# Optimization experiments

Measured on AMD Instinct MI355X. Metric: run time of the kernel, lower is better.

## Reference

```python
import jax, jax.numpy as jnp
import numpy as np

# Module config (matches init_kwargs shape_data=[8,32,32], pow=1, spde_type='adv_diff')
N_T, N_Y, N_X = 8, 32, 32
N = N_Y * N_X            # nb_nodes
DX = DY = DT = 1.0


def build_A(kappa, m1, m2, h11, h12, h22):
    """Dense [N,N] advection-diffusion operator A = kappa^2 I + m.grad - div(H grad),
    central differences on the n_y x n_x grid, zero-Dirichlet boundary (9-pt stencil).
    All coefficient inputs are [N] vectors (node-wise)."""
    ii, jj = jnp.divmod(jnp.arange(N), N_X)   # ii: y index, jj: x index
    rows = jnp.arange(N)
    A = jnp.zeros((N, N), dtype=kappa.dtype)
    # center
    A = A.at[rows, rows].add(kappa ** 2 + 2.0 * h11 / DX**2 + 2.0 * h22 / DY**2)

    def add(A, di, dj, coef):
        vi, vj = ii + di, jj + dj
        valid = (vi >= 0) & (vi < N_Y) & (vj >= 0) & (vj < N_X)
        cols = jnp.clip(vi, 0, N_Y - 1) * N_X + jnp.clip(vj, 0, N_X - 1)
        return A.at[rows, cols].add(jnp.where(valid, coef, 0.0))

    A = add(A, 0, +1, -h11 / DX**2 + m1 / (2.0 * DX))
    A = add(A, 0, -1, -h11 / DX**2 - m1 / (2.0 * DX))
    A = add(A, +1, 0, -h22 / DY**2 + m2 / (2.0 * DY))
    A = add(A, -1, 0, -h22 / DY**2 - m2 / (2.0 * DY))
    cxy = h12 / (2.0 * DX * DY)    # cross term -2*H12*u_xy with /(4 dx dy) stencil
    A = add(A, +1, +1, -cxy)
    A = add(A, -1, -1, -cxy)
    A = add(A, +1, -1, +cxy)
    A = add(A, -1, +1, +cxy)
    return A


def _forward(kappa, m, H, tau):
    n_b = kappa.shape[0]
    # reorder field params to [n_b, n_t, N]
    kap = jnp.moveaxis(kappa[:, 0], -1, 1)
    m1 = jnp.moveaxis(m[:, 0], -1, 1)
    m2 = jnp.moveaxis(m[:, 1], -1, 1)
    h11 = jnp.moveaxis(H[:, 0, 0], -1, 1)
    h12 = jnp.moveaxis(H[:, 0, 1], -1, 1)
    h22 = jnp.moveaxis(H[:, 1, 1], -1, 1)
    tau_ = jnp.moveaxis(tau[:, 0], -1, 1)

    flat = lambda a: a.reshape(n_b * N_T, N)
    A = jax.vmap(build_A)(flat(kap), flat(m1), flat(m2), flat(h11), flat(h12), flat(h22))
    A = A.reshape(n_b, N_T, N, N)                 # B = A since pow == 1

    eye = jnp.eye(N, dtype=A.dtype)
    M = eye + DT * A                               # inv_M_k = I + dt*B_k, [n_b,n_t,N,N]
    w = DT / (tau_ ** 2)                           # Qs_tilde_k = diag(dt / tau_k^2)

    WM = w[..., :, None] * M                       # diag(w_k) @ M_k
    P = jnp.einsum('btij,btik->btjk', M, WM)       # M_k^T diag(w_k) M_k

    # diagonal blocks: D_k = P_k + diag(w_{k+1}) for k < n_t-1; D_{n_t-1} = P_{n_t-1}
    w_next = jnp.concatenate([w[:, 1:], jnp.zeros_like(w[:, :1])], axis=1)
    D = P + w_next[..., :, None] * eye

    # sub-diagonal block (k, k-1) = -M_k^T diag(w_k), k = 1..n_t-1 (0-block padded at front)
    zblk = jnp.zeros((n_b, 1, N, N), dtype=A.dtype)
    lower = jnp.concatenate([zblk, -jnp.swapaxes(WM[:, 1:], -1, -2)], axis=1)
    # super-diagonal block (k, k+1) = -diag(w_{k+1}) M_{k+1}, k = 0..n_t-2 (0-block at end)
    upper = jnp.concatenate([-WM[:, 1:], zblk], axis=1)

    # block-tridiagonal precision Q, packed as [n_b, 3(diag,lower,upper), n_t, N, N]
    return jnp.stack([D, lower, upper], axis=1)


def setup_inputs() -> dict:
    key = jax.random.key(0)
    ks = jax.random.split(key, 4)
    n_b = 2
    kappa = 0.1 + 0.9 * jax.random.uniform(ks[0], (n_b, 1, N, N_T), dtype=jnp.float32)
    m = 0.2 * jax.random.normal(ks[1], (n_b, 2, N, N_T), dtype=jnp.float32)
    H = jax.random.uniform(ks[2], (n_b, 2, 2, N, N_T), dtype=jnp.float32)
    H = H.at[:, 0, 1].multiply(0.2)
    H = H.at[:, 1, 0].set(H[:, 0, 1])              # symmetric diffusion tensor
    tau = 0.5 + jax.random.uniform(ks[3], (n_b, 1, N, N_T), dtype=jnp.float32)
    return {"kappa": kappa, "m": m, "H": H, "tau": tau}


def reference(kappa, m, H, tau):
    return _forward(kappa, m, H, tau)
```

## Files before the change

kernel.cpp:

```cpp
#include <hip/hip_runtime.h>

#define NT 8
#define NY 32
#define NX 32
#define NN 1024

__device__ __forceinline__ void node_coefs(const float* __restrict__ kap,
                                           const float* __restrict__ m,
                                           const float* __restrict__ H,
                                           const float* __restrict__ tau,
                                           int b, int node, int tc,
                                           int iy, int ix,
                                           float* c , float& w) {
    const int base = node * NT + tc;
    const float kp  = kap[(b * NN) * NT + base];
    const float m1  = m[((b * 2 + 0) * NN) * NT + base];
    const float m2  = m[((b * 2 + 1) * NN) * NT + base];
    const float h11 = H[((b * 4 + 0) * NN) * NT + base];
    const float h12 = H[((b * 4 + 1) * NN) * NT + base];
    const float h22 = H[((b * 4 + 3) * NN) * NT + base];
    const float tv  = tau[(b * NN) * NT + base];
    w = 1.0f / (tv * tv);

    const float cxy = 0.5f * h12;
    const bool ym = iy > 0, yp = iy < NY - 1;
    const bool xm = ix > 0, xp = ix < NX - 1;

    c[4] = 1.0f + kp * kp + 2.0f * h11 + 2.0f * h22;
    c[0] = (ym && xm) ? -cxy               : 0.0f;
    c[1] =  ym        ? (-h22 - 0.5f * m2) : 0.0f;
    c[2] = (ym && xp) ?  cxy               : 0.0f;
    c[3] =  xm        ? (-h11 - 0.5f * m1) : 0.0f;
    c[5] =  xp        ? (-h11 + 0.5f * m1) : 0.0f;
    c[6] = (yp && xm) ?  cxy               : 0.0f;
    c[7] =  yp        ? (-h22 + 0.5f * m2) : 0.0f;
    c[8] = (yp && xp) ? -cxy               : 0.0f;
}

__global__ __launch_bounds__(256) void spde_kernel(const float* __restrict__ kap,
                                                   const float* __restrict__ m,
                                                   const float* __restrict__ H,
                                                   const float* __restrict__ tau,
                                                   float* __restrict__ out) {
    __shared__ float sc[9][9];
    __shared__ float sw[9];
    __shared__ float valsD[25];
    __shared__ float valsL[9];
    __shared__ float valsU[9];

    const int gb = blockIdx.x;
    const int j  = gb & (NN - 1);
    const int bt = gb >> 10;
    const int t  = bt & 7;
    const int b  = bt >> 3;
    const int jy = j >> 5, jx = j & 31;
    const int tid = threadIdx.x;

    if (tid < 9) {
        const int ey = tid / 3 - 1, ex = tid % 3 - 1;
        const int iy = jy + ey, ix = jx + ex;
        float c[9];
        float w = 0.0f;
        if (iy >= 0 && iy < NY && ix >= 0 && ix < NX) {
            node_coefs(kap, m, H, tau, b, iy * NX + ix, t, iy, ix, c, w);
        } else {
            #pragma unroll
            for (int q = 0; q < 9; ++q) c[q] = 0.0f;
        }
        #pragma unroll
        for (int q = 0; q < 9; ++q) sc[tid][q] = c[q];
        sw[tid] = w;
    }
    __syncthreads();

    if (tid < 25) {
        const int dy = tid / 5 - 2, dx = tid % 5 - 2;
        float acc = 0.0f;
        #pragma unroll
        for (int d = 0; d < 9; ++d) {
            const int ey = d / 3 - 1, ex = d % 3 - 1;
            const int r2y = dy - ey, r2x = dx - ex;
            if (r2y >= -1 && r2y <= 1 && r2x >= -1 && r2x <= 1) {
                acc += sw[d] * sc[d][8 - d] * sc[d][(r2y + 1) * 3 + (r2x + 1)];
            }
        }
        if (tid == 12 && t < NT - 1) {
            const float tv = tau[((size_t)b * NN + j) * NT + (t + 1)];
            acc += 1.0f / (tv * tv);
        }
        valsD[tid] = acc;
    } else if (tid >= 64 && tid < 73) {
        const int d = tid - 64;
        valsL[d] = -sw[d] * sc[d][8 - d];
    } else if (tid >= 73 && tid < 82) {
        const int q = tid - 73;
        valsU[q] = -sw[4] * sc[4][q];
    }
    __syncthreads();

    const int cy  = tid >> 3;
    const int cx0 = (tid & 7) * 4;
    const int ddy = cy - jy;
    float4* const outq = (float4*)out;
    const size_t rowq = ((size_t)j << 8) + tid;
    const size_t matD = ((size_t)(b * 3 + 0) * NT + t) << 18;
    const size_t matL = ((size_t)(b * 3 + 1) * NT + t) << 18;

    {
        float4 v = make_float4(0.f, 0.f, 0.f, 0.f);
        if (ddy >= -2 && ddy <= 2) {
            float* vp = &v.x;
            const float* wrow = &valsD[(ddy + 2) * 5 + 2];
            #pragma unroll
            for (int qq = 0; qq < 4; ++qq) {
                const int ddx = cx0 + qq - jx;
                if (ddx >= -2 && ddx <= 2) vp[qq] = wrow[ddx];
            }
        }
        outq[matD + rowq] = v;
    }
    {
        float4 v = make_float4(0.f, 0.f, 0.f, 0.f);
        if (t > 0 && ddy >= -1 && ddy <= 1) {
            float* vp = &v.x;
            const float* wrow = &valsL[(ddy + 1) * 3 + 1];
            #pragma unroll
            for (int qq = 0; qq < 4; ++qq) {
                const int ddx = cx0 + qq - jx;
                if (ddx >= -1 && ddx <= 1) vp[qq] = wrow[ddx];
            }
        }
        outq[matL + rowq] = v;
    }
    if (t >= 1) {
        const size_t matU = ((size_t)(b * 3 + 2) * NT + (t - 1)) << 18;
        float4 v = make_float4(0.f, 0.f, 0.f, 0.f);
        if (ddy >= -1 && ddy <= 1) {
            float* vp = &v.x;
            const float* wrow = &valsU[(ddy + 1) * 3 + 1];
            #pragma unroll
            for (int qq = 0; qq < 4; ++qq) {
                const int ddx = cx0 + qq - jx;
                if (ddx >= -1 && ddx <= 1) vp[qq] = wrow[ddx];
            }
        }
        outq[matU + rowq] = v;
        if (t == NT - 1) {
            const size_t matU7 = ((size_t)(b * 3 + 2) * NT + 7) << 18;
            outq[matU7 + rowq] = make_float4(0.f, 0.f, 0.f, 0.f);
        }
    }
}

extern "C" void kernel_launch(void* const* d_in, const int* in_sizes, int n_in,
                              void* d_out, int out_size, void* d_ws, size_t ws_size,
                              hipStream_t stream) {
    const float* kap = (const float*)d_in[0];
    const float* m   = (const float*)d_in[1];
    const float* H   = (const float*)d_in[2];
    const float* tau = (const float*)d_in[3];
    float* out = (float*)d_out;

    const int n_b = in_sizes[0] / (NN * NT);
    const int grid = n_b * NT * NN;
    spde_kernel<<<grid, 256, 0, stream>>>(kap, m, H, tau, out);
}
```

Baseline: 199.3 us.

## Process a full grid row per block to reuse neighbor coefficients

Each block now handles a whole row of 32 output rows (one jy slab) instead of a single matrix row, loading a 3x32 halo of node coefficients once into shared memory. Per-row stencil weights are computed for all 32 columns and each thread writes 32 float4 stores per matrix in a loop. This cuts the launch count by 32x and removes the redundant coefficient loads repeated by neighboring blocks, in exchange for fewer blocks (512) and more serial store work per thread. The U block for t=0 now writes zeros into slot NT-1 through the same loop.

```diff
diff --git a/kernel.cpp b/kernel.cpp
--- a/kernel.cpp
+++ b/kernel.cpp
@@ -37,64 +37,63 @@
     c[8] = (yp && xp) ? -cxy               : 0.0f;
 }
 
-__global__ __launch_bounds__(256) void spde_kernel(const float* __restrict__ kap,
+__global__ __launch_bounds__(256) void slab_kernel(const float* __restrict__ kap,
                                                    const float* __restrict__ m,
                                                    const float* __restrict__ H,
                                                    const float* __restrict__ tau,
                                                    float* __restrict__ out) {
-    __shared__ float sc[9][9];
-    __shared__ float sw[9];
-    __shared__ float valsD[25];
-    __shared__ float valsL[9];
-    __shared__ float valsU[9];
+    __shared__ float sc[96][9];
+    __shared__ float sw[96];
+    __shared__ float valsD[32][25];
+    __shared__ float valsU[32][9];
 
-    const int gb = blockIdx.x;
-    const int j  = gb & (NN - 1);
-    const int bt = gb >> 10;
-    const int t  = bt & 7;
-    const int b  = bt >> 3;
-    const int jy = j >> 5, jx = j & 31;
+    const int blk = blockIdx.x;
+    const int jy = blk & 31;
+    const int t  = (blk >> 5) & 7;
+    const int b  = blk >> 8;
     const int tid = threadIdx.x;
 
-    if (tid < 9) {
-        const int ey = tid / 3 - 1, ex = tid % 3 - 1;
-        const int iy = jy + ey, ix = jx + ex;
-        float c[9];
+    if (tid < 96) {
+        const int r = tid >> 5;
+        const int c = tid & 31;
+        const int iy = jy - 1 + r;
+        float cf[9];
         float w = 0.0f;
-        if (iy >= 0 && iy < NY && ix >= 0 && ix < NX) {
-            node_coefs(kap, m, H, tau, b, iy * NX + ix, t, iy, ix, c, w);
+        if (iy >= 0 && iy < NY) {
+            node_coefs(kap, m, H, tau, b, iy * NX + c, t, iy, c, cf, w);
         } else {
             #pragma unroll
-            for (int q = 0; q < 9; ++q) c[q] = 0.0f;
+            for (int q = 0; q < 9; ++q) cf[q] = 0.0f;
         }
         #pragma unroll
-        for (int q = 0; q < 9; ++q) sc[tid][q] = c[q];
+        for (int q = 0; q < 9; ++q) sc[tid][q] = cf[q];
         sw[tid] = w;
     }
     __syncthreads();
 
-    if (tid < 25) {
-        const int dy = tid / 5 - 2, dx = tid % 5 - 2;
+    for (int e = tid; e < 32 * 25; e += 256) {
+        const int jx = e / 25, widx = e % 25;
+        const int dy = widx / 5 - 2, dx = widx % 5 - 2;
         float acc = 0.0f;
         #pragma unroll
         for (int d = 0; d < 9; ++d) {
             const int ey = d / 3 - 1, ex = d % 3 - 1;
             const int r2y = dy - ey, r2x = dx - ex;
-            if (r2y >= -1 && r2y <= 1 && r2x >= -1 && r2x <= 1) {
-                acc += sw[d] * sc[d][8 - d] * sc[d][(r2y + 1) * 3 + (r2x + 1)];
-            }
+            if (r2y < -1 || r2y > 1 || r2x < -1 || r2x > 1) continue;
+            const int col = jx + ex;
+            if ((unsigned)col >= 32u) continue;
+            const int i = (ey + 1) * 32 + col;
+            acc += sw[i] * sc[i][8 - d] * sc[i][(r2y + 1) * 3 + (r2x + 1)];
         }
-        if (tid == 12 && t < NT - 1) {
-            const float tv = tau[((size_t)b * NN + j) * NT + (t + 1)];
+        if (widx == 12 && t < NT - 1) {
+            const float tv = tau[((size_t)b * NN + jy * NX + jx) * NT + (t + 1)];
             acc += 1.0f / (tv * tv);
         }
-        valsD[tid] = acc;
-    } else if (tid >= 64 && tid < 73) {
-        const int d = tid - 64;
-        valsL[d] = -sw[d] * sc[d][8 - d];
-    } else if (tid >= 73 && tid < 82) {
-        const int q = tid - 73;
-        valsU[q] = -sw[4] * sc[4][q];
+        valsD[jx][widx] = acc;
+    }
+    for (int e = tid; e < 32 * 9; e += 256) {
+        const int jx = e / 9, off = e % 9;
+        valsU[jx][off] = -sw[32 + jx] * sc[32 + jx][off];
     }
     __syncthreads();
 
@@ -102,52 +101,73 @@
     const int cx0 = (tid & 7) * 4;
     const int ddy = cy - jy;
     float4* const outq = (float4*)out;
-    const size_t rowq = ((size_t)j << 8) + tid;
-    const size_t matD = ((size_t)(b * 3 + 0) * NT + t) << 18;
-    const size_t matL = ((size_t)(b * 3 + 1) * NT + t) << 18;
+    const size_t rowbase = ((size_t)jy << 13) + tid;
 
     {
-        float4 v = make_float4(0.f, 0.f, 0.f, 0.f);
-        if (ddy >= -2 && ddy <= 2) {
-            float* vp = &v.x;
-            const float* wrow = &valsD[(ddy + 2) * 5 + 2];
+        float4* p = outq + (((size_t)(b * 3 + 0) * NT + t) << 18) + rowbase;
+        const bool act = (ddy >= -2 && ddy <= 2);
+        const float* wrow = &valsD[0][(ddy + 2) * 5 + 2];
+        #pragma unroll 4
+        for (int jx = 0; jx < 32; ++jx) {
+            float4 v = make_float4(0.f, 0.f, 0.f, 0.f);
+            if (act) {
+                float* vp = &v.x;
+                #pragma unroll
+                for (int qq = 0; qq < 4; ++qq) {
+                    const int ddx = cx0 + qq - jx;
+                    if (ddx >= -2 && ddx <= 2) vp[qq] = wrow[jx * 25 + ddx];
+                }
+            }
+            p[(size_t)jx << 8] = v;
+        }
+    }
+
+    {
+        float4* p = outq + (((size_t)(b * 3 + 1) * NT + t) << 18) + rowbase;
+        const bool act = (t > 0) && (ddy >= -1 && ddy <= 1);
+        float Lv[12];
+        if (act) {
             #pragma unroll
             for (int qq = 0; qq < 4; ++qq) {
-                const int ddx = cx0 + qq - jx;
-                if (ddx >= -2 && ddx <= 2) vp[qq] = wrow[ddx];
+                const int k = (ddy + 1) * 32 + cx0 + qq;
+                const float wk = sw[k];
+                #pragma unroll
+                for (int xi = 0; xi < 3; ++xi)
+                    Lv[qq * 3 + xi] = -wk * sc[k][8 - ((ddy + 1) * 3 + xi)];
             }
         }
-        outq[matD + rowq] = v;
+        #pragma unroll 4
+        for (int jx = 0; jx < 32; ++jx) {
+            float4 v = make_float4(0.f, 0.f, 0.f, 0.f);
+            if (act) {
+                float* vp = &v.x;
+                #pragma unroll
+                for (int qq = 0; qq < 4; ++qq) {
+                    const int ddx = cx0 + qq - jx;
+                    if (ddx >= -1 && ddx <= 1) vp[qq] = Lv[qq * 3 + ddx + 1];
+                }
+            }
+            p[(size_t)jx << 8] = v;
+        }
     }
+
     {
-        float4 v = make_float4(0.f, 0.f, 0.f, 0.f);
-        if (t > 0 && ddy >= -1 && ddy <= 1) {
-            float* vp = &v.x;
-            const float* wrow = &valsL[(ddy + 1) * 3 + 1];
-            #pragma unroll
-            for (int qq = 0; qq < 4; ++qq) {
-                const int ddx = cx0 + qq - jx;
-                if (ddx >= -1 && ddx <= 1) vp[qq] = wrow[ddx];
+        const int ut = (t >= 1) ? (t - 1) : (NT - 1);
+        float4* p = outq + (((size_t)(b * 3 + 2) * NT + ut) << 18) + rowbase;
+        const bool act = (t >= 1) && (ddy >= -1 && ddy <= 1);
+        #pragma unroll 4
+        for (int jx = 0; jx < 32; ++jx) {
+            float4 v = make_float4(0.f, 0.f, 0.f, 0.f);
+            if (act) {
+                float* vp = &v.x;
+                #pragma unroll
+                for (int qq = 0; qq < 4; ++qq) {
+                    const int ddx = cx0 + qq - jx;
+                    if (ddx >= -1 && ddx <= 1)
+                        vp[qq] = valsU[jx][(ddy + 1) * 3 + ddx + 1];
+                }
             }
-        }
-        outq[matL + rowq] = v;
-    }
-    if (t >= 1) {
-        const size_t matU = ((size_t)(b * 3 + 2) * NT + (t - 1)) << 18;
-        float4 v = make_float4(0.f, 0.f, 0.f, 0.f);
-        if (ddy >= -1 && ddy <= 1) {
-            float* vp = &v.x;
-            const float* wrow = &valsU[(ddy + 1) * 3 + 1];
-            #pragma unroll
-            for (int qq = 0; qq < 4; ++qq) {
-                const int ddx = cx0 + qq - jx;
-                if (ddx >= -1 && ddx <= 1) vp[qq] = wrow[ddx];
-            }
-        }
-        outq[matU + rowq] = v;
-        if (t == NT - 1) {
-            const size_t matU7 = ((size_t)(b * 3 + 2) * NT + 7) << 18;
-            outq[matU7 + rowq] = make_float4(0.f, 0.f, 0.f, 0.f);
+            p[(size_t)jx << 8] = v;
         }
     }
 }
@@ -162,6 +182,6 @@
     float* out = (float*)d_out;
 
     const int n_b = in_sizes[0] / (NN * NT);
-    const int grid = n_b * NT * NN;
-    spde_kernel<<<grid, 256, 0, stream>>>(kap, m, H, tau, out);
+    const int grid = n_b * NT * NY;
+    slab_kernel<<<grid, 256, 0, stream>>>(kap, m, H, tau, out);
 }
```

Result: slower. 210.7 us (+5.7%).
